# Kernel tuning notes

Measured on AMD Instinct MI355X. Metric: run time of the kernel, lower is better.

## Reference

```python
import jax, jax.numpy as jnp
import numpy as np

N = 16_777_216  # total elements
B = 16_384      # number of segments (graphs/batches)
EPS = 1e-12


def setup_inputs() -> dict:
    key = jax.random.key(0)
    k1, k2, k3 = jax.random.split(key, 3)
    preds = jax.random.normal(k1, (N,), dtype=jnp.float32)
    target = jax.random.normal(k2, (N,), dtype=jnp.float32)
    batch_map = jnp.sort(jax.random.randint(k3, (N,), 0, B, dtype=jnp.int64))
    return {"preds": preds, "target": target, "batch_map": batch_map}


def reference(preds, target, batch_map):
    # per-segment squared norms and dot product (three scatter-sums in torch)
    seg = lambda v: jax.ops.segment_sum(v, batch_map, num_segments=B,
                                        indices_are_sorted=True)
    preds_norm = jnp.sqrt(seg(preds * preds))      # [B]
    target_norm = jnp.sqrt(seg(target * target))   # [B]
    dot_product = seg(preds * target)              # [B]
    cosine = dot_product / jnp.maximum(preds_norm * target_norm, EPS)
    return jnp.mean(1.0 - cosine)
```

## Files before the change

kernel.cpp:

```cpp
#include <hip/hip_runtime.h>

#define NSEG 16384
#define EPS  1e-12f

__global__ void bsearch_kernel(const int* __restrict__ map,
                               int* __restrict__ start, int n) {
    int b = blockIdx.x * blockDim.x + threadIdx.x;
    if (b > NSEG) return;
    int est = b << 10;
    int wlo = est - 20000; if (wlo < 0) wlo = 0;
    int whi = est + 20000; if (whi > n) whi = n;
    int lo = wlo, hi = whi;
    while (lo < hi) { int mid = (lo + hi) >> 1; if (map[mid] < b) lo = mid + 1; else hi = mid; }
    bool bad = (lo == wlo && wlo > 0 && map[wlo - 1] >= b) ||
               (lo == whi && whi < n && map[whi] < b);
    if (bad) {
        lo = 0; hi = n;
        while (lo < hi) { int mid = (lo + hi) >> 1; if (map[mid] < b) lo = mid + 1; else hi = mid; }
    }
    start[b] = lo;
}

#define REDUCE3(x, y, z)                              \
    do {                                              \
        _Pragma("unroll")                             \
        for (int off_ = 32; off_ > 0; off_ >>= 1) {   \
            x += __shfl_down(x, off_);                \
            y += __shfl_down(y, off_);                \
            z += __shfl_down(z, off_);                \
        }                                             \
    } while (0)

#define COL(pe, te, eidx)                                                       \
    { const float px_ = (pe), tx_ = (te);                                       \
      const float cxx_ = px_ * px_, cyy_ = tx_ * tx_, cxy_ = px_ * tx_;         \
      const bool i0_ = (eidx) < bb1_;                                           \
      const bool i2_ = (eidx) >= bb2_;                                          \
      a0 += i0_ ? cxx_ : 0.f; c0 += i0_ ? cyy_ : 0.f; d0 += i0_ ? cxy_ : 0.f;   \
      a2 += i2_ ? cxx_ : 0.f; c2 += i2_ ? cyy_ : 0.f; d2 += i2_ ? cxy_ : 0.f;   \
      const bool i1_ = !i0_ && !i2_;                                            \
      a1 += i1_ ? cxx_ : 0.f; c1 += i1_ ? cyy_ : 0.f; d1 += i1_ ? cxy_ : 0.f; }

#define DO_HALF(P, T, HBASE, MH, SFIRST, B1, B2, CC)                            \
    do {                                                                        \
        float a0=0,c0=0,d0=0, a1=0,c1=0,d1=0, a2=0,c2=0,d2=0;                   \
        const int bb1_ = (B1), bb2_ = (B2);                                     \
        const int hend_ = (HBASE) + 1024;                                       \
        _Pragma("unroll")                                                       \
        for (int g_ = 0; g_ < 4; ++g_) {                                        \
            const float4 pv = P[g_], tv = T[g_];                                \
            const int G_  = (HBASE) + g_ * 256;                                 \
            const int Ge_ = G_ + 256;                                           \
            if (Ge_ <= bb1_) {                                                  \
                a0 += pv.x*pv.x + pv.y*pv.y + pv.z*pv.z + pv.w*pv.w;            \
                c0 += tv.x*tv.x + tv.y*tv.y + tv.z*tv.z + tv.w*tv.w;            \
                d0 += pv.x*tv.x + pv.y*tv.y + pv.z*tv.z + pv.w*tv.w;            \
            } else if (G_ >= bb1_ && Ge_ <= bb2_) {                             \
                a1 += pv.x*pv.x + pv.y*pv.y + pv.z*pv.z + pv.w*pv.w;            \
                c1 += tv.x*tv.x + tv.y*tv.y + tv.z*tv.z + tv.w*tv.w;            \
                d1 += pv.x*tv.x + pv.y*tv.y + pv.z*tv.z + pv.w*tv.w;            \
            } else if (G_ >= bb2_) {                                            \
                a2 += pv.x*pv.x + pv.y*pv.y + pv.z*pv.z + pv.w*pv.w;            \
                c2 += tv.x*tv.x + tv.y*tv.y + tv.z*tv.z + tv.w*tv.w;            \
                d2 += pv.x*tv.x + pv.y*tv.y + pv.z*tv.z + pv.w*tv.w;            \
            } else {                                                            \
                const int e0_ = (HBASE) + (g_ * 64 + lane) * 4;                 \
                COL(pv.x, tv.x, e0_ + 0)                                        \
                COL(pv.y, tv.y, e0_ + 1)                                        \
                COL(pv.z, tv.z, e0_ + 2)                                        \
                COL(pv.w, tv.w, e0_ + 3)                                        \
            }                                                                   \
        }                                                                       \
        const int nloc_ = (bb1_ < hend_) + (bb2_ < hend_);                      \
        REDUCE3(a0, c0, d0);                                                    \
        if (nloc_ >= 1) REDUCE3(a1, c1, d1);                                    \
        if (nloc_ >= 2) REDUCE3(a2, c2, d2);                                    \
        if (lane == 0) {                                                        \
            wb[(MH) * 3 + ((CC) - ((SFIRST) >> 10))] = make_float4(a0, c0, d0, 0.f); \
            if (nloc_ >= 1) wb[((MH) + 1) * 3] = make_float4(a1, c1, d1, 0.f);  \
            if (nloc_ >= 2) wb[((MH) + 2) * 3] = make_float4(a2, c2, d2, 0.f);  \
        }                                                                       \
    } while (0)

__global__ __launch_bounds__(256) void seg_main(const float4* __restrict__ p4,
                                                const float4* __restrict__ t4,
                                                const int* __restrict__ start,
                                                float4* __restrict__ wb) {
    const int lane = threadIdx.x & 63;
    const int wid  = __builtin_amdgcn_readfirstlane(threadIdx.x >> 6);
    const int w     = blockIdx.x * 4 + wid;
    const int ebase = w << 11;
    const int vbase = w << 9;

    const int base_id = (ebase >> 10) - 20;
    int gidx = base_id + lane;
    gidx = gidx < 0 ? 0 : (gidx > NSEG ? NSEG : gidx);
    const int sv = start[gidx];

    float4 PA[4], TA[4], PB[4], TB[4];
    #pragma unroll
    for (int k = 0; k < 4; ++k) PA[k] = p4[vbase + k * 64 + lane];
    #pragma unroll
    for (int k = 0; k < 4; ++k) TA[k] = t4[vbase + k * 64 + lane];
    #pragma unroll
    for (int k = 0; k < 4; ++k) PB[k] = p4[vbase + 256 + k * 64 + lane];
    #pragma unroll
    for (int k = 0; k < 4; ++k) TB[k] = t4[vbase + 256 + k * 64 + lane];

    const unsigned long long m0 = __ballot(sv <= ebase);
    const int k0 = 63 - __builtin_clzll(m0);
    const unsigned long long m1 = __ballot(sv <= ebase + 1024);
    const int k1 = 63 - __builtin_clzll(m1);

    const int mh0 = base_id + k0;
    const int mh1 = base_id + k1;
    const int s00 = __builtin_amdgcn_readlane(sv, k0);
    const int b01 = __builtin_amdgcn_readlane(sv, k0 + 1 > 63 ? 63 : k0 + 1);
    const int b02 = __builtin_amdgcn_readlane(sv, k0 + 2 > 63 ? 63 : k0 + 2);
    const int s10 = __builtin_amdgcn_readlane(sv, k1);
    const int b11 = __builtin_amdgcn_readlane(sv, k1 + 1 > 63 ? 63 : k1 + 1);
    const int b12 = __builtin_amdgcn_readlane(sv, k1 + 2 > 63 ? 63 : k1 + 2);

    DO_HALF(PA, TA, ebase,        mh0, s00, b01, b02, (w << 1));
    DO_HALF(PB, TB, ebase + 1024, mh1, s10, b11, b12, (w << 1) + 1);
}

__global__ void finalize1(const float4* __restrict__ wb,
                          const int* __restrict__ start,
                          float* __restrict__ part) {
    float local = 0.0f;
    for (int s = blockIdx.x * blockDim.x + threadIdx.x; s < NSEG;
         s += gridDim.x * blockDim.x) {
        const int s0 = start[s], s1 = start[s + 1];
        float cosv = 0.0f;
        if (s1 > s0) {
            float4 v = wb[s * 3];
            const int r0 = s0 >> 10, r1 = (s1 - 1) >> 10;
            if (r1 > r0)     { float4 u = wb[s * 3 + 1]; v.x += u.x; v.y += u.y; v.z += u.z; }
            if (r1 > r0 + 1) { float4 u = wb[s * 3 + 2]; v.x += u.x; v.y += u.y; v.z += u.z; }
            cosv = v.z / fmaxf(sqrtf(v.x) * sqrtf(v.y), EPS);
        }
        local += 1.0f - cosv;
    }
    #pragma unroll
    for (int off = 32; off > 0; off >>= 1) local += __shfl_down(local, off);
    __shared__ float wsum[4];
    const int wd = threadIdx.x >> 6;
    if ((threadIdx.x & 63) == 0) wsum[wd] = local;
    __syncthreads();
    if (threadIdx.x == 0)
        part[blockIdx.x] = wsum[0] + wsum[1] + wsum[2] + wsum[3];
}

__global__ void finalize2(const float* __restrict__ part,
                          float* __restrict__ out, int npart) {
    float local = (threadIdx.x < npart) ? part[threadIdx.x] : 0.0f;
    #pragma unroll
    for (int off = 32; off > 0; off >>= 1) local += __shfl_down(local, off);
    if (threadIdx.x == 0) out[0] = local / (float)NSEG;
}

extern "C" void kernel_launch(void* const* d_in, const int* in_sizes, int n_in,
                              void* d_out, int out_size, void* d_ws, size_t ws_size,
                              hipStream_t stream) {
    const float4* p = (const float4*)d_in[0];
    const float4* t = (const float4*)d_in[1];
    const int*    s = (const int*)d_in[2];
    const int n = in_sizes[0];

    int*    start = (int*)d_ws;
    float4* wb    = (float4*)((char*)d_ws + 65552);
    float*  part  = (float*)((char*)d_ws + 65552 + 786432);

    bsearch_kernel<<<65, 256, 0, stream>>>(s, start, n);
    seg_main<<<2048, 256, 0, stream>>>(p, t, start, wb);
    finalize1<<<64, 256, 0, stream>>>(wb, start, part);
    finalize2<<<1, 64, 0, stream>>>(part, (float*)d_out, 64);
}
```

Baseline: 38.31 us.

## Process four chunks per wave with double-buffered loads and DPP reductions

Each wave now handles four 1024-element chunks instead of two, double-buffering register loads so the next chunk's loads are issued while the current one is reduced, and the grid is halved to match. The shuffle-based wave reductions are replaced with DPP row operations plus row broadcasts, with the result read from lane 63. This aims to hide memory latency and cut reduction cost, at the price of fewer waves in flight and more sequential work per wave.

```diff
diff --git a/kernel.cpp b/kernel.cpp
--- a/kernel.cpp
+++ b/kernel.cpp
@@ -21,65 +21,94 @@
     start[b] = lo;
 }
 
-#define REDUCE3(x, y, z)                              \
-    do {                                              \
-        _Pragma("unroll")                             \
-        for (int off_ = 32; off_ > 0; off_ >>= 1) {   \
-            x += __shfl_down(x, off_);                \
-            y += __shfl_down(y, off_);                \
-            z += __shfl_down(z, off_);                \
-        }                                             \
+__device__ __forceinline__ float dpp_add(float x, int ctrl);
+#define DPP_ADD_IMPL(CTRL)                                                     \
+    __device__ __forceinline__ float dpp_add_##CTRL(float x) {                 \
+        int y = __builtin_amdgcn_update_dpp(0, __float_as_int(x), CTRL,        \
+                                            0xf, 0xf, true);                   \
+        return x + __int_as_float(y);                                          \
+    }
+DPP_ADD_IMPL(0x111)
+DPP_ADD_IMPL(0x112)
+DPP_ADD_IMPL(0x114)
+DPP_ADD_IMPL(0x118)
+DPP_ADD_IMPL(0x142)
+DPP_ADD_IMPL(0x143)
+
+#define DPPRED3(x, y, z)                                         \
+    do {                                                         \
+        x = dpp_add_0x111(x); y = dpp_add_0x111(y); z = dpp_add_0x111(z); \
+        x = dpp_add_0x112(x); y = dpp_add_0x112(y); z = dpp_add_0x112(z); \
+        x = dpp_add_0x114(x); y = dpp_add_0x114(y); z = dpp_add_0x114(z); \
+        x = dpp_add_0x118(x); y = dpp_add_0x118(y); z = dpp_add_0x118(z); \
+        x = dpp_add_0x142(x); y = dpp_add_0x142(y); z = dpp_add_0x142(z); \
+        x = dpp_add_0x143(x); y = dpp_add_0x143(y); z = dpp_add_0x143(z); \
     } while (0)
 
-#define COL(pe, te, eidx)                                                       \
-    { const float px_ = (pe), tx_ = (te);                                       \
-      const float cxx_ = px_ * px_, cyy_ = tx_ * tx_, cxy_ = px_ * tx_;         \
-      const bool i0_ = (eidx) < bb1_;                                           \
-      const bool i2_ = (eidx) >= bb2_;                                          \
-      a0 += i0_ ? cxx_ : 0.f; c0 += i0_ ? cyy_ : 0.f; d0 += i0_ ? cxy_ : 0.f;   \
-      a2 += i2_ ? cxx_ : 0.f; c2 += i2_ ? cyy_ : 0.f; d2 += i2_ ? cxy_ : 0.f;   \
-      const bool i1_ = !i0_ && !i2_;                                            \
-      a1 += i1_ ? cxx_ : 0.f; c1 += i1_ ? cyy_ : 0.f; d1 += i1_ ? cxy_ : 0.f; }
+#define LOADC(P, T, CIDX)                                                      \
+    do {                                                                       \
+        const int vb_ = (CIDX) << 8;                                           \
+        _Pragma("unroll")                                                      \
+        for (int k_ = 0; k_ < 4; ++k_) P[k_] = p4[vb_ + k_ * 64 + lane];       \
+        _Pragma("unroll")                                                      \
+        for (int k_ = 0; k_ < 4; ++k_) T[k_] = t4[vb_ + k_ * 64 + lane];       \
+    } while (0)
 
-#define DO_HALF(P, T, HBASE, MH, SFIRST, B1, B2, CC)                            \
-    do {                                                                        \
-        float a0=0,c0=0,d0=0, a1=0,c1=0,d1=0, a2=0,c2=0,d2=0;                   \
-        const int bb1_ = (B1), bb2_ = (B2);                                     \
-        const int hend_ = (HBASE) + 1024;                                       \
-        _Pragma("unroll")                                                       \
-        for (int g_ = 0; g_ < 4; ++g_) {                                        \
-            const float4 pv = P[g_], tv = T[g_];                                \
-            const int G_  = (HBASE) + g_ * 256;                                 \
-            const int Ge_ = G_ + 256;                                           \
-            if (Ge_ <= bb1_) {                                                  \
-                a0 += pv.x*pv.x + pv.y*pv.y + pv.z*pv.z + pv.w*pv.w;            \
-                c0 += tv.x*tv.x + tv.y*tv.y + tv.z*tv.z + tv.w*tv.w;            \
-                d0 += pv.x*tv.x + pv.y*tv.y + pv.z*tv.z + pv.w*tv.w;            \
-            } else if (G_ >= bb1_ && Ge_ <= bb2_) {                             \
-                a1 += pv.x*pv.x + pv.y*pv.y + pv.z*pv.z + pv.w*pv.w;            \
-                c1 += tv.x*tv.x + tv.y*tv.y + tv.z*tv.z + tv.w*tv.w;            \
-                d1 += pv.x*tv.x + pv.y*tv.y + pv.z*tv.z + pv.w*tv.w;            \
-            } else if (G_ >= bb2_) {                                            \
-                a2 += pv.x*pv.x + pv.y*pv.y + pv.z*pv.z + pv.w*pv.w;            \
-                c2 += tv.x*tv.x + tv.y*tv.y + tv.z*tv.z + tv.w*tv.w;            \
-                d2 += pv.x*tv.x + pv.y*tv.y + pv.z*tv.z + pv.w*tv.w;            \
-            } else {                                                            \
-                const int e0_ = (HBASE) + (g_ * 64 + lane) * 4;                 \
-                COL(pv.x, tv.x, e0_ + 0)                                        \
-                COL(pv.y, tv.y, e0_ + 1)                                        \
-                COL(pv.z, tv.z, e0_ + 2)                                        \
-                COL(pv.w, tv.w, e0_ + 3)                                        \
-            }                                                                   \
-        }                                                                       \
-        const int nloc_ = (bb1_ < hend_) + (bb2_ < hend_);                      \
-        REDUCE3(a0, c0, d0);                                                    \
-        if (nloc_ >= 1) REDUCE3(a1, c1, d1);                                    \
-        if (nloc_ >= 2) REDUCE3(a2, c2, d2);                                    \
-        if (lane == 0) {                                                        \
-            wb[(MH) * 3 + ((CC) - ((SFIRST) >> 10))] = make_float4(a0, c0, d0, 0.f); \
-            if (nloc_ >= 1) wb[((MH) + 1) * 3] = make_float4(a1, c1, d1, 0.f);  \
-            if (nloc_ >= 2) wb[((MH) + 2) * 3] = make_float4(a2, c2, d2, 0.f);  \
-        }                                                                       \
+#define COLX(pe, te, eidx)                                                     \
+    { const float px_ = (pe), tx_ = (te);                                      \
+      const float cxx_ = px_ * px_, cyy_ = tx_ * tx_, cxy_ = px_ * tx_;        \
+      const bool i0_ = (eidx) < b1_;                                           \
+      const bool i2_ = (eidx) >= b2_;                                          \
+      q0 += i0_ ? cxx_ : 0.f; r0 += i0_ ? cyy_ : 0.f; u0 += i0_ ? cxy_ : 0.f;  \
+      q2 += i2_ ? cxx_ : 0.f; r2 += i2_ ? cyy_ : 0.f; u2 += i2_ ? cxy_ : 0.f;  \
+      const bool i1_ = !i0_ && !i2_;                                           \
+      q1 += i1_ ? cxx_ : 0.f; r1 += i1_ ? cyy_ : 0.f; u1 += i1_ ? cxy_ : 0.f; }
+
+#define DO_CHUNK(P, T, CIDX)                                                   \
+    do {                                                                       \
+        const int hb_ = (CIDX) << 10;                                          \
+        const unsigned long long mm_ = __ballot(sv <= hb_);                    \
+        const int kk_ = 63 - __builtin_clzll(mm_);                             \
+        const int mh_ = base_id + kk_;                                         \
+        const int sA_ = __builtin_amdgcn_readlane(sv, kk_);                    \
+        const int k1_ = kk_ + 1 > 63 ? 63 : kk_ + 1;                           \
+        const int k2_ = kk_ + 2 > 63 ? 63 : kk_ + 2;                           \
+        const int b1_ = __builtin_amdgcn_readlane(sv, k1_);                    \
+        const int b2_ = __builtin_amdgcn_readlane(sv, k2_);                    \
+        float q0=0,r0=0,u0=0, q1=0,r1=0,u1=0, q2=0,r2=0,u2=0;                  \
+        _Pragma("unroll")                                                      \
+        for (int g_ = 0; g_ < 4; ++g_) {                                       \
+            const float4 pv = P[g_], tv = T[g_];                               \
+            const int G_ = hb_ + g_ * 256, Ge_ = G_ + 256;                     \
+            if (Ge_ <= b1_) {                                                  \
+                q0 += pv.x*pv.x + pv.y*pv.y + pv.z*pv.z + pv.w*pv.w;           \
+                r0 += tv.x*tv.x + tv.y*tv.y + tv.z*tv.z + tv.w*tv.w;           \
+                u0 += pv.x*tv.x + pv.y*tv.y + pv.z*tv.z + pv.w*tv.w;           \
+            } else if (G_ >= b1_ && Ge_ <= b2_) {                              \
+                q1 += pv.x*pv.x + pv.y*pv.y + pv.z*pv.z + pv.w*pv.w;           \
+                r1 += tv.x*tv.x + tv.y*tv.y + tv.z*tv.z + tv.w*tv.w;           \
+                u1 += pv.x*tv.x + pv.y*tv.y + pv.z*tv.z + pv.w*tv.w;           \
+            } else if (G_ >= b2_) {                                            \
+                q2 += pv.x*pv.x + pv.y*pv.y + pv.z*pv.z + pv.w*pv.w;           \
+                r2 += tv.x*tv.x + tv.y*tv.y + tv.z*tv.z + tv.w*tv.w;           \
+                u2 += pv.x*tv.x + pv.y*tv.y + pv.z*tv.z + pv.w*tv.w;           \
+            } else {                                                           \
+                const int e0_ = hb_ + (g_ * 64 + lane) * 4;                    \
+                COLX(pv.x, tv.x, e0_ + 0)                                      \
+                COLX(pv.y, tv.y, e0_ + 1)                                      \
+                COLX(pv.z, tv.z, e0_ + 2)                                      \
+                COLX(pv.w, tv.w, e0_ + 3)                                      \
+            }                                                                  \
+        }                                                                      \
+        const int nloc_ = (b1_ < hb_ + 1024) + (b2_ < hb_ + 1024);             \
+        DPPRED3(q0, r0, u0);                                                   \
+        if (nloc_ >= 1) DPPRED3(q1, r1, u1);                                   \
+        if (nloc_ >= 2) DPPRED3(q2, r2, u2);                                   \
+        if (lane == 63) {                                                      \
+            wb[mh_ * 3 + ((CIDX) - (sA_ >> 10))] = make_float4(q0, r0, u0, 0.f); \
+            if (nloc_ >= 1) wb[(mh_ + 1) * 3] = make_float4(q1, r1, u1, 0.f);  \
+            if (nloc_ >= 2) wb[(mh_ + 2) * 3] = make_float4(q2, r2, u2, 0.f);  \
+        }                                                                      \
     } while (0)
 
 __global__ __launch_bounds__(256) void seg_main(const float4* __restrict__ p4,
@@ -87,42 +116,24 @@
                                                 const int* __restrict__ start,
                                                 float4* __restrict__ wb) {
     const int lane = threadIdx.x & 63;
-    const int wid  = __builtin_amdgcn_readfirstlane(threadIdx.x >> 6);
-    const int w     = blockIdx.x * 4 + wid;
-    const int ebase = w << 11;
-    const int vbase = w << 9;
+    const int wv   = (blockIdx.x << 2) + (threadIdx.x >> 6);
+    const int c0   = wv << 2;
 
-    const int base_id = (ebase >> 10) - 20;
+    const int base_id = c0 - 20;
     int gidx = base_id + lane;
     gidx = gidx < 0 ? 0 : (gidx > NSEG ? NSEG : gidx);
     const int sv = start[gidx];
 
     float4 PA[4], TA[4], PB[4], TB[4];
-    #pragma unroll
-    for (int k = 0; k < 4; ++k) PA[k] = p4[vbase + k * 64 + lane];
-    #pragma unroll
-    for (int k = 0; k < 4; ++k) TA[k] = t4[vbase + k * 64 + lane];
-    #pragma unroll
-    for (int k = 0; k < 4; ++k) PB[k] = p4[vbase + 256 + k * 64 + lane];
-    #pragma unroll
-    for (int k = 0; k < 4; ++k) TB[k] = t4[vbase + 256 + k * 64 + lane];
+    LOADC(PA, TA, c0);
+    LOADC(PB, TB, c0 + 1);
 
-    const unsigned long long m0 = __ballot(sv <= ebase);
-    const int k0 = 63 - __builtin_clzll(m0);
-    const unsigned long long m1 = __ballot(sv <= ebase + 1024);
-    const int k1 = 63 - __builtin_clzll(m1);
-
-    const int mh0 = base_id + k0;
-    const int mh1 = base_id + k1;
-    const int s00 = __builtin_amdgcn_readlane(sv, k0);
-    const int b01 = __builtin_amdgcn_readlane(sv, k0 + 1 > 63 ? 63 : k0 + 1);
-    const int b02 = __builtin_amdgcn_readlane(sv, k0 + 2 > 63 ? 63 : k0 + 2);
-    const int s10 = __builtin_amdgcn_readlane(sv, k1);
-    const int b11 = __builtin_amdgcn_readlane(sv, k1 + 1 > 63 ? 63 : k1 + 1);
-    const int b12 = __builtin_amdgcn_readlane(sv, k1 + 2 > 63 ? 63 : k1 + 2);
-
-    DO_HALF(PA, TA, ebase,        mh0, s00, b01, b02, (w << 1));
-    DO_HALF(PB, TB, ebase + 1024, mh1, s10, b11, b12, (w << 1) + 1);
+    DO_CHUNK(PA, TA, c0);
+    LOADC(PA, TA, c0 + 2);
+    DO_CHUNK(PB, TB, c0 + 1);
+    LOADC(PB, TB, c0 + 3);
+    DO_CHUNK(PA, TA, c0 + 2);
+    DO_CHUNK(PB, TB, c0 + 3);
 }
 
 __global__ void finalize1(const float4* __restrict__ wb,
@@ -173,7 +184,7 @@
     float*  part  = (float*)((char*)d_ws + 65552 + 786432);
 
     bsearch_kernel<<<65, 256, 0, stream>>>(s, start, n);
-    seg_main<<<2048, 256, 0, stream>>>(p, t, start, wb);
+    seg_main<<<1024, 256, 0, stream>>>(p, t, start, wb);
     finalize1<<<64, 256, 0, stream>>>(wb, start, part);
     finalize2<<<1, 64, 0, stream>>>(part, (float*)d_out, 64);
 }
```

Result: faster. 37.28 us (-2.7%).
